# Kernel tuning notes

Measured on AMD Instinct MI355X. Metric: run time of the kernel, lower is better.

## Reference

```python
import jax, jax.numpy as jnp
import numpy as np

WS = (4, 4, 4)  # window shape (wd, wh, ww)
EPS = 1e-5


def _layernorm(x, g, b):
    mu = jnp.mean(x, axis=-1, keepdims=True)
    var = jnp.mean(jnp.square(x - mu), axis=-1, keepdims=True)
    return (x - mu) * jax.lax.rsqrt(var + EPS) * g + b


def _partition(x, ws):
    # x: [B, D, H, W, C] -> [num_windows, wd*wh*ww, C]
    B, D, H, W, C = x.shape
    x = x.reshape(B, D // ws[0], ws[0], H // ws[1], ws[1], W // ws[2], ws[2], C)
    x = jnp.transpose(x, (0, 1, 3, 5, 2, 4, 6, 7))
    return x.reshape(-1, ws[0] * ws[1] * ws[2], C)


def _merge(win, shape, ws):
    B, D, H, W, C = shape
    x = win.reshape(B, D // ws[0], H // ws[1], W // ws[2], ws[0], ws[1], ws[2], C)
    x = jnp.transpose(x, (0, 1, 4, 2, 5, 3, 6, 7))
    return x.reshape(B, D, H, W, C)


def setup_inputs() -> dict:
    key = jax.random.key(0)
    ks = jax.random.split(key, 8)
    B, D, H, W, C = 2, 32, 64, 64, 96
    nh, kd = 4, 24
    s = 0.02
    return {
        "x": jax.random.normal(ks[0], (B, D, H, W, C), jnp.float32),
        "ln1_g": jnp.ones((C,), jnp.float32),
        "ln1_b": jnp.zeros((C,), jnp.float32),
        "wq": jax.random.normal(ks[1], (C, nh, kd), jnp.float32) * s,
        "bq": jnp.zeros((nh, kd), jnp.float32),
        "wk": jax.random.normal(ks[2], (C, nh, kd), jnp.float32) * s,
        "bk": jnp.zeros((nh, kd), jnp.float32),
        "wv": jax.random.normal(ks[3], (C, nh, kd), jnp.float32) * s,
        "bv": jnp.zeros((nh, kd), jnp.float32),
        "wo": jax.random.normal(ks[4], (nh, kd, C), jnp.float32) * s,
        "bo": jnp.zeros((C,), jnp.float32),
        "ln2_g": jnp.ones((C,), jnp.float32),
        "ln2_b": jnp.zeros((C,), jnp.float32),
        "w1": jax.random.normal(ks[5], (C, 4 * C), jnp.float32) * s,
        "b1": jnp.zeros((4 * C,), jnp.float32),
        "w2": jax.random.normal(ks[6], (4 * C, C), jnp.float32) * s,
        "b2": jnp.zeros((C,), jnp.float32),
    }


def reference(x, ln1_g, ln1_b, wq, bq, wk, bk, wv, bv, wo, bo,
              ln2_g, ln2_b, w1, b1, w2, b2):
    shape = x.shape  # [B, D, H, W, C]; dims chosen divisible by WS -> pad is a no-op
    kd = wq.shape[-1]
    shortcut = x
    h = _layernorm(x, ln1_g, ln1_b)
    win = _partition(h, WS)  # [n, L, C], L = 64
    # Keras MultiHeadAttention (inference, dropout off)
    q = jnp.einsum("nlc,chd->nlhd", win, wq) + bq
    k = jnp.einsum("nlc,chd->nlhd", win, wk) + bk
    v = jnp.einsum("nlc,chd->nlhd", win, wv) + bv
    scores = jnp.einsum("nlhd,nmhd->nhlm", q, k) / jnp.sqrt(jnp.float32(kd))
    attn = jax.nn.softmax(scores, axis=-1)
    o = jnp.einsum("nhlm,nmhd->nlhd", attn, v)
    out = jnp.einsum("nlhd,hdc->nlc", o, wo) + bo
    x = shortcut + _merge(out, shape, WS)
    shortcut = x
    h = _layernorm(x, ln2_g, ln2_b)
    h = jax.nn.gelu(h @ w1 + b1, approximate=False)  # TF keras 'gelu' is exact
    h = h @ w2 + b2
    return shortcut + h
```

## Files before the change

kernel.cpp:

```cpp
#include <hip/hip_runtime.h>
#include <hip/hip_bf16.h>

typedef __attribute__((ext_vector_type(8))) short short8;
typedef __attribute__((ext_vector_type(4))) short short4b;
typedef __attribute__((ext_vector_type(4))) float f32x4;
typedef unsigned short ushort_t;

#define NTOK 262144

__device__ __forceinline__ ushort_t f2bf(float f){
  __hip_bfloat16 h = __float2bfloat16(f);
  return *reinterpret_cast<ushort_t*>(&h);
}
__device__ __forceinline__ float bf2f(ushort_t u){
  union { unsigned int i; float f; } v; v.i = ((unsigned int)u) << 16; return v.f;
}
__device__ __forceinline__ float fast_rcp(float x){
  float r; asm("v_rcp_f32 %0, %1" : "=v"(r) : "v"(x)); return r;
}
__device__ __forceinline__ float gelu_f(float x){
  float x2 = x * x;
  float z = x * fmaf(0.0356774081f, x2, 0.7978845608f);
  float e = __expf(2.0f * z);
  float t = 1.0f - 2.0f * fast_rcp(e + 1.0f);
  return 0.5f * x * (1.0f + t);
}
__device__ __forceinline__ void bar_lds(){
  asm volatile("s_waitcnt lgkmcnt(0)" ::: "memory");
  __builtin_amdgcn_s_barrier();
}
__device__ __forceinline__ void gl_lds16(const ushort_t* g, ushort_t* l){
  __builtin_amdgcn_global_load_lds(
      (const __attribute__((address_space(1))) void*)g,
      (__attribute__((address_space(3))) void*)l, 16, 0, 0);
}

template<int NT>
__device__ __forceinline__ void stage_w(const ushort_t* __restrict__ src,
                                        int src_stride, ushort_t (*dst)[104], int tid)
{
  #pragma unroll
  for (int it = 0; it < (1248 + NT - 1) / NT; ++it) {
    int u = tid + it * NT;
    if (u < 1248) {
      int row = u / 13, c16 = u % 13;
      const ushort_t* sp = src + row * src_stride + ((c16 == 12) ? 0 : c16 * 8);
      gl_lds16(sp, &dst[0][0] + (size_t)(u & ~63) * 8);
    }
  }
}

__global__ __launch_bounds__(256) void prep_kernel(
    const float* __restrict__ wq, const float* __restrict__ wk, const float* __restrict__ wv,
    const float* __restrict__ wo, const float* __restrict__ w1, const float* __restrict__ w2,
    const float* __restrict__ bq, const float* __restrict__ bk, const float* __restrict__ bv,
    ushort_t* __restrict__ Wqkv, ushort_t* __restrict__ Wo,
    ushort_t* __restrict__ W1, ushort_t* __restrict__ W2, float* __restrict__ biasq)
{
  const float qs = 0.20412414523193150818f;
  int i = blockIdx.x * 256 + threadIdx.x;
  if (i < 27648) {
    int j = i / 96, c = i % 96;
    int s = j / 96, rem = j % 96;
    const float* src = (s == 0) ? wq : (s == 1) ? wk : wv;
    float val = src[c * 96 + rem];
    if (s == 0) val *= qs;
    Wqkv[j * 96 + c] = f2bf(val);
  } else if (i < 36864) {
    int ii = i - 27648;
    int c = ii / 96, hd = ii % 96;
    Wo[ii] = f2bf(wo[hd * 96 + c]);
  } else if (i < 73728) {
    int ii = i - 36864;
    int j = ii / 96, c = ii % 96;
    W1[ii] = f2bf(w1[c * 384 + j]);
  } else if (i < 110592) {
    int ii = i - 73728;
    int c = ii / 384, j = ii % 384;
    W2[ii] = f2bf(w2[j * 96 + c]);
  } else if (i < 110880) {
    int j = i - 110592;
    int s = j / 96, rem = j % 96;
    const float* src = (s == 0) ? bq : (s == 1) ? bk : bv;
    float val = src[rem];
    if (s == 0) val *= qs;
    biasq[j] = val;
  }
}

__global__ __launch_bounds__(256, 2) void fat_kernel(
    const float* __restrict__ x, const float* __restrict__ g, const float* __restrict__ b,
    const ushort_t* __restrict__ Wqkv, const float* __restrict__ biasq,
    const ushort_t* __restrict__ Wo, const float* __restrict__ bo,
    ushort_t* __restrict__ x2b)
{
  __shared__ ushort_t regionA[19968];
  __shared__ ushort_t Vt[4][32][72];
  __shared__ ushort_t Ws[96][104];
  ushort_t (*hbt)[104]   = reinterpret_cast<ushort_t(*)[104]>(regionA);
  ushort_t (*QK)[208]    = reinterpret_cast<ushort_t(*)[208]>(regionA + 64 * 104);
  ushort_t (*Pb)[64][72] = reinterpret_cast<ushort_t(*)[64][72]>(regionA);
  ushort_t (*O_lds)[104] = reinterpret_cast<ushort_t(*)[104]>(regionA);

  int tid = threadIdx.x;
  int n = blockIdx.x;
  int wq_ = n & 15, hq = (n >> 4) & 15, rest = n >> 8;
  int dq = rest & 7, bb_ = rest >> 3;
  int base = bb_ * 131072 + dq * 16384 + hq * 256 + wq_ * 4;
  #define TOK(s) (base + ((s) >> 4) * 4096 + (((s) >> 2) & 3) * 64 + ((s) & 3))

  stage_w<256>(Wqkv, 96, Ws, tid);

  {
    int s = tid >> 2, qr = tid & 3;
    const float* xp = x + (size_t)TOK(s) * 96 + qr * 24;
    f32x4 v[6];
    float sm = 0.f, sq = 0.f;
    #pragma unroll
    for (int i = 0; i < 6; i++) {
      v[i] = *reinterpret_cast<const f32x4*>(xp + i * 4);
      #pragma unroll
      for (int j = 0; j < 4; j++) { sm += v[i][j]; sq += v[i][j] * v[i][j]; }
    }
    sm += __shfl_xor(sm, 1); sq += __shfl_xor(sq, 1);
    sm += __shfl_xor(sm, 2); sq += __shfl_xor(sq, 2);
    float mean = sm * (1.0f / 96.0f);
    float var  = sq * (1.0f / 96.0f) - mean * mean;
    float rstd = rsqrtf(var + 1e-5f);
    #pragma unroll
    for (int i8 = 0; i8 < 3; i8++) {
      short8 pk;
      #pragma unroll
      for (int j = 0; j < 8; j++) {
        int c = qr * 24 + i8 * 8 + j;
        pk[j] = (short)f2bf((v[(i8 * 8 + j) >> 2][(i8 * 8 + j) & 3] - mean) * rstd * g[c] + b[c]);
      }
      *reinterpret_cast<short8*>(&hbt[s][qr * 24 + i8 * 8]) = pk;
    }
  }
  __syncthreads();

  int w = tid >> 6, lane = tid & 63, g16 = lane >> 4, l15 = lane & 15;
  short8 af[3];
  #pragma unroll
  for (int ks = 0; ks < 3; ks++)
    af[ks] = *reinterpret_cast<const short8*>(&hbt[w * 16 + l15][ks * 32 + g16 * 8]);

  for (int grp = 0; grp < 3; ++grp) {
    f32x4 acc[6];
    #pragma unroll
    for (int j = 0; j < 6; j++) acc[j] = (f32x4){0.f, 0.f, 0.f, 0.f};
    #pragma unroll
    for (int j = 0; j < 6; j++)
      #pragma unroll
      for (int ks = 0; ks < 3; ks++) {
        short8 wfr = *reinterpret_cast<const short8*>(&Ws[j * 16 + l15][ks * 32 + g16 * 8]);
        acc[j] = __builtin_amdgcn_mfma_f32_16x16x32_bf16(wfr, af[ks], acc[j], 0, 0, 0);
      }
    bar_lds();
    if (grp < 2) stage_w<256>(Wqkv + (grp + 1) * 9216, 96, Ws, tid);
    else         stage_w<256>(Wo, 96, Ws, tid);
    if (grp < 2) {
      #pragma unroll
      for (int j = 0; j < 6; j++) {
        int c0 = grp * 96 + j * 16 + g16 * 4;
        f32x4 bb4 = *reinterpret_cast<const f32x4*>(&biasq[c0]);
        unsigned lo = (unsigned)f2bf(acc[j][0] + bb4[0]) | ((unsigned)f2bf(acc[j][1] + bb4[1]) << 16);
        unsigned hi = (unsigned)f2bf(acc[j][2] + bb4[2]) | ((unsigned)f2bf(acc[j][3] + bb4[3]) << 16);
        uint2 pk; pk.x = lo; pk.y = hi;
        *reinterpret_cast<uint2*>(&QK[w * 16 + l15][c0]) = pk;
      }
    } else {
      #pragma unroll
      for (int j = 0; j < 6; j++) {
        int c0 = j * 16 + g16 * 4;
        f32x4 bb4 = *reinterpret_cast<const f32x4*>(&biasq[192 + c0]);
        #pragma unroll
        for (int r = 0; r < 4; r++) {
          int vcol = c0 + r;
          int h2 = vcol / 24, d2 = vcol - h2 * 24;
          Vt[h2][d2][w * 16 + l15] = f2bf(acc[j][r] + bb4[r]);
        }
      }
    }
    __syncthreads();
  }

  int h = w;
  short8 kf[4], qf[4];
  const short8 z8 = {0, 0, 0, 0, 0, 0, 0, 0};
  #pragma unroll
  for (int i = 0; i < 4; i++) {
    qf[i] = (g16 < 3) ? *(const short8*)&QK[i * 16 + l15][h * 24 + g16 * 8]      : z8;
    kf[i] = (g16 < 3) ? *(const short8*)&QK[i * 16 + l15][96 + h * 24 + g16 * 8] : z8;
  }
  f32x4 st[4][4];
  #pragma unroll
  for (int tm = 0; tm < 4; tm++)
    #pragma unroll
    for (int tn = 0; tn < 4; tn++)
      st[tm][tn] = __builtin_amdgcn_mfma_f32_16x16x32_bf16(kf[tm], qf[tn],
                    (f32x4){0.f, 0.f, 0.f, 0.f}, 0, 0, 0);
  bar_lds();

  #pragma unroll
  for (int tn = 0; tn < 4; tn++) {
    float m = st[0][tn][0];
    #pragma unroll
    for (int tm = 0; tm < 4; tm++)
      #pragma unroll
      for (int r = 0; r < 4; r++) m = fmaxf(m, st[tm][tn][r]);
    m = fmaxf(m, __shfl_xor(m, 16));
    m = fmaxf(m, __shfl_xor(m, 32));
    float sum = 0.f;
    #pragma unroll
    for (int tm = 0; tm < 4; tm++)
      #pragma unroll
      for (int r = 0; r < 4; r++) {
        float e = __expf(st[tm][tn][r] - m);
        st[tm][tn][r] = e;
        sum += e;
      }
    sum += __shfl_xor(sum, 16);
    sum += __shfl_xor(sum, 32);
    float inv = fast_rcp(sum);
    int q = tn * 16 + l15;
    #pragma unroll
    for (int tm = 0; tm < 4; tm++) {
      unsigned lo = (unsigned)f2bf(st[tm][tn][0] * inv) | ((unsigned)f2bf(st[tm][tn][1] * inv) << 16);
      unsigned hi = (unsigned)f2bf(st[tm][tn][2] * inv) | ((unsigned)f2bf(st[tm][tn][3] * inv) << 16);
      uint2 pk; pk.x = lo; pk.y = hi;
      *(uint2*)&Pb[h][q][tm * 16 + g16 * 4] = pk;
    }
  }

  f32x4 oacc[4][2];
  #pragma unroll
  for (int qt = 0; qt < 4; qt++)
    #pragma unroll
    for (int dt = 0; dt < 2; dt++) oacc[qt][dt] = (f32x4){0.f, 0.f, 0.f, 0.f};
  #pragma unroll
  for (int ks = 0; ks < 2; ks++) {
    short8 vb[2];
    #pragma unroll
    for (int dt = 0; dt < 2; dt++)
      vb[dt] = *(const short8*)&Vt[h][dt * 16 + l15][ks * 32 + g16 * 8];
    #pragma unroll
    for (int qt = 0; qt < 4; qt++) {
      short8 pa = *(const short8*)&Pb[h][qt * 16 + l15][ks * 32 + g16 * 8];
      #pragma unroll
      for (int dt = 0; dt < 2; dt++)
        oacc[qt][dt] = __builtin_amdgcn_mfma_f32_16x16x32_bf16(pa, vb[dt], oacc[qt][dt], 0, 0, 0);
    }
  }

  __syncthreads();
  #pragma unroll
  for (int qt = 0; qt < 4; qt++)
    #pragma unroll
    for (int dt = 0; dt < 2; dt++) {
      int d = dt * 16 + l15;
      if (d < 24) {
        #pragma unroll
        for (int r = 0; r < 4; r++)
          O_lds[qt * 16 + g16 * 4 + r][h * 24 + d] = f2bf(oacc[qt][dt][r]);
      }
    }
  __syncthreads();

  f32x4 pacc[6];
  #pragma unroll
  for (int nt = 0; nt < 6; nt++) pacc[nt] = (f32x4){0.f, 0.f, 0.f, 0.f};
  #pragma unroll
  for (int ks = 0; ks < 3; ks++) {
    short8 pa = *(const short8*)&O_lds[w * 16 + l15][ks * 32 + g16 * 8];
    #pragma unroll
    for (int nt = 0; nt < 6; nt++) {
      short8 wb = *reinterpret_cast<const short8*>(&Ws[nt * 16 + l15][ks * 32 + g16 * 8]);
      pacc[nt] = __builtin_amdgcn_mfma_f32_16x16x32_bf16(pa, wb, pacc[nt], 0, 0, 0);
    }
  }
  #pragma unroll
  for (int nt = 0; nt < 6; nt++) {
    int col = nt * 16 + l15;
    float bs = bo[col];
    #pragma unroll
    for (int r = 0; r < 4; r++) {
      int s2 = w * 16 + g16 * 4 + r;
      size_t t = (size_t)TOK(s2);
      float v = pacc[nt][r] + bs + x[t * 96 + col];
      x2b[t * 96 + col] = f2bf(v);
    }
  }
  #undef TOK
}

__device__ __forceinline__ void ln_to_lds_b(const ushort_t* __restrict__ xrow_base,
    const float* __restrict__ gg, const float* __restrict__ bb,
    ushort_t (*hbt)[104], int tid)
{
  int row = tid >> 1, half = tid & 1;
  const ushort_t* xp = xrow_base + (size_t)row * 96 + half * 48;
  short8 vv[6];
  #pragma unroll
  for (int i = 0; i < 6; i++) vv[i] = *reinterpret_cast<const short8*>(xp + i * 8);
  float v[48];
  float s = 0.f, sq = 0.f;
  #pragma unroll
  for (int i = 0; i < 6; i++)
    #pragma unroll
    for (int j = 0; j < 8; j++) {
      float f = bf2f((ushort_t)vv[i][j]);
      v[i * 8 + j] = f; s += f; sq += f * f;
    }
  s  += __shfl_xor(s, 1);
  sq += __shfl_xor(sq, 1);
  float mean = s * (1.0f / 96.0f);
  float var  = sq * (1.0f / 96.0f) - mean * mean;
  float rstd = rsqrtf(var + 1e-5f);
  #pragma unroll
  for (int i8 = 0; i8 < 6; i8++) {
    short8 pk;
    #pragma unroll
    for (int j = 0; j < 8; j++) {
      int c = half * 48 + i8 * 8 + j;
      pk[j] = (short)f2bf((v[i8 * 8 + j] - mean) * rstd * gg[c] + bb[c]);
    }
    *reinterpret_cast<short8*>(&hbt[row][half * 48 + i8 * 8]) = pk;
  }
}

__global__ __launch_bounds__(256, 3) void mlp2_kernel(
    const ushort_t* __restrict__ x2b, const float* __restrict__ g, const float* __restrict__ b,
    const ushort_t* __restrict__ W1t, const float* __restrict__ b1,
    const ushort_t* __restrict__ W2t, const float* __restrict__ b2,
    float* __restrict__ out)
{
  __shared__ ushort_t smem[128][104];
  __shared__ ushort_t Ws[96][104];
  int tid = threadIdx.x;
  size_t r0 = (size_t)blockIdx.x * 128;

  stage_w<256>(W1t, 96, Ws, tid);
  ln_to_lds_b(x2b + r0 * 96, g, b, smem, tid);
  __syncthreads();

  int w = tid >> 6, lane = tid & 63, g16 = lane >> 4, l15 = lane & 15;
  short8 af[2][3];
  #pragma unroll
  for (int mi = 0; mi < 2; mi++)
    #pragma unroll
    for (int ks = 0; ks < 3; ks++)
      af[mi][ks] = *reinterpret_cast<const short8*>(&smem[w * 32 + mi * 16 + l15][ks * 32 + g16 * 8]);

  f32x4 oacc[6][2];
  #pragma unroll
  for (int nt = 0; nt < 6; nt++) { oacc[nt][0] = (f32x4){0.f,0.f,0.f,0.f}; oacc[nt][1] = (f32x4){0.f,0.f,0.f,0.f}; }

  for (int cc = 0; cc < 4; ++cc) {
    f32x4 acc[6][2];
    #pragma unroll
    for (int nt = 0; nt < 6; nt++) { acc[nt][0] = (f32x4){0.f,0.f,0.f,0.f}; acc[nt][1] = (f32x4){0.f,0.f,0.f,0.f}; }
    #pragma unroll
    for (int nt = 0; nt < 6; nt++)
      #pragma unroll
      for (int ks = 0; ks < 3; ks++) {
        short8 wfr = *reinterpret_cast<const short8*>(&Ws[nt * 16 + l15][ks * 32 + g16 * 8]);
        acc[nt][0] = __builtin_amdgcn_mfma_f32_16x16x32_bf16(wfr, af[0][ks], acc[nt][0], 0, 0, 0);
        acc[nt][1] = __builtin_amdgcn_mfma_f32_16x16x32_bf16(wfr, af[1][ks], acc[nt][1], 0, 0, 0);
      }
    bar_lds();
    stage_w<256>(W2t + cc * 96, 384, Ws, tid);
    #pragma unroll
    for (int nt = 0; nt < 6; nt++) {
      f32x4 bb4 = *reinterpret_cast<const f32x4*>(&b1[cc * 96 + nt * 16 + g16 * 4]);
      #pragma unroll
      for (int mi = 0; mi < 2; mi++) {
        float g0 = gelu_f(acc[nt][mi][0] + bb4[0]);
        float g1 = gelu_f(acc[nt][mi][1] + bb4[1]);
        float g2 = gelu_f(acc[nt][mi][2] + bb4[2]);
        float g3 = gelu_f(acc[nt][mi][3] + bb4[3]);
        unsigned lo = (unsigned)f2bf(g0) | ((unsigned)f2bf(g1) << 16);
        unsigned hi = (unsigned)f2bf(g2) | ((unsigned)f2bf(g3) << 16);
        uint2 pk; pk.x = lo; pk.y = hi;
        *reinterpret_cast<uint2*>(&smem[w * 32 + mi * 16 + l15][nt * 16 + g16 * 4]) = pk;
      }
    }
    short8 a2[2][3];
    #pragma unroll
    for (int mi = 0; mi < 2; mi++)
      #pragma unroll
      for (int ks = 0; ks < 3; ks++)
        a2[mi][ks] = *reinterpret_cast<const short8*>(&smem[w * 32 + mi * 16 + l15][ks * 32 + g16 * 8]);
    __syncthreads();
    #pragma unroll
    for (int nt = 0; nt < 6; nt++)
      #pragma unroll
      for (int ks = 0; ks < 3; ks++) {
        short8 wfr = *reinterpret_cast<const short8*>(&Ws[nt * 16 + l15][ks * 32 + g16 * 8]);
        oacc[nt][0] = __builtin_amdgcn_mfma_f32_16x16x32_bf16(wfr, a2[0][ks], oacc[nt][0], 0, 0, 0);
        oacc[nt][1] = __builtin_amdgcn_mfma_f32_16x16x32_bf16(wfr, a2[1][ks], oacc[nt][1], 0, 0, 0);
      }
    if (cc < 3) {
      bar_lds();
      stage_w<256>(W1t + (cc + 1) * 96 * 96, 96, Ws, tid);
      __syncthreads();
    }
  }

  #pragma unroll
  for (int nt = 0; nt < 6; nt++) {
    int c0 = nt * 16 + g16 * 4;
    f32x4 bb4 = *reinterpret_cast<const f32x4*>(&b2[c0]);
    #pragma unroll
    for (int mi = 0; mi < 2; mi++) {
      size_t row = r0 + w * 32 + mi * 16 + l15;
      short4b rr = *reinterpret_cast<const short4b*>(&x2b[row * 96 + c0]);
      f32x4 o;
      #pragma unroll
      for (int r = 0; r < 4; r++) o[r] = oacc[nt][mi][r] + bb4[r] + bf2f((ushort_t)rr[r]);
      *reinterpret_cast<f32x4*>(&out[row * 96 + c0]) = o;
    }
  }
}

extern "C" void kernel_launch(void* const* d_in, const int* in_sizes, int n_in,
                              void* d_out, int out_size, void* d_ws, size_t ws_size,
                              hipStream_t stream)
{
  (void)in_sizes; (void)n_in; (void)out_size; (void)ws_size;
  const float* x    = (const float*)d_in[0];
  const float* ln1g = (const float*)d_in[1];
  const float* ln1b = (const float*)d_in[2];
  const float* wq   = (const float*)d_in[3];
  const float* bq   = (const float*)d_in[4];
  const float* wk   = (const float*)d_in[5];
  const float* bk   = (const float*)d_in[6];
  const float* wv   = (const float*)d_in[7];
  const float* bv   = (const float*)d_in[8];
  const float* wo   = (const float*)d_in[9];
  const float* bo   = (const float*)d_in[10];
  const float* ln2g = (const float*)d_in[11];
  const float* ln2b = (const float*)d_in[12];
  const float* w1   = (const float*)d_in[13];
  const float* b1   = (const float*)d_in[14];
  const float* w2   = (const float*)d_in[15];
  const float* b2   = (const float*)d_in[16];

  char* ws = (char*)d_ws;
  ushort_t* x2b  = (ushort_t*)(ws);
  char* wsw      = ws + 50331648;
  ushort_t* Wqkv = (ushort_t*)(wsw);
  ushort_t* Wo   = (ushort_t*)(wsw + 55296);
  ushort_t* W1   = (ushort_t*)(wsw + 55296 + 18432);
  ushort_t* W2   = (ushort_t*)(wsw + 55296 + 18432 + 73728);
  float*    biasq= (float*)   (wsw + 55296 + 18432 + 73728 + 73728);

  prep_kernel<<<434, 256, 0, stream>>>(wq, wk, wv, wo, w1, w2, bq, bk, bv,
                                       Wqkv, Wo, W1, W2, biasq);
  fat_kernel<<<4096, 256, 0, stream>>>(x, ln1g, ln1b, Wqkv, biasq, Wo, bo, x2b);
  mlp2_kernel<<<NTOK / 128, 256, 0, stream>>>(x2b, ln2g, ln2b, W1, b1, W2, b2, (float*)d_out);
}
```

Measured before the change: 197.6 us.

## Double-buffer MLP weight tiles in LDS with vmcnt-based prefetch barriers

The MLP kernel now keeps separate LDS buffers for the W1 and W2 chunks and prefetches the next chunk with async global-to-LDS loads while the current GEMM runs. Barriers wait on partial vmcnt counts instead of draining all loads. Biases are staged in LDS, and the fat kernel's QK row stride is padded to 216. This aims to hide weight-load latency and cut barrier stalls, at the cost of more LDS, which lowers occupancy from 3 to 2 blocks per CU.

```diff
diff --git a/kernel.cpp b/kernel.cpp
--- a/kernel.cpp
+++ b/kernel.cpp
@@ -28,6 +28,17 @@
 __device__ __forceinline__ void bar_lds(){
   asm volatile("s_waitcnt lgkmcnt(0)" ::: "memory");
   __builtin_amdgcn_s_barrier();
+  __builtin_amdgcn_sched_barrier(0);
+}
+__device__ __forceinline__ void bar_cnt5(){
+  asm volatile("s_waitcnt vmcnt(5) lgkmcnt(0)" ::: "memory");
+  __builtin_amdgcn_s_barrier();
+  __builtin_amdgcn_sched_barrier(0);
+}
+__device__ __forceinline__ void bar_cnt0(){
+  asm volatile("s_waitcnt vmcnt(0) lgkmcnt(0)" ::: "memory");
+  __builtin_amdgcn_s_barrier();
+  __builtin_amdgcn_sched_barrier(0);
 }
 __device__ __forceinline__ void gl_lds16(const ushort_t* g, ushort_t* l){
   __builtin_amdgcn_global_load_lds(
@@ -47,6 +58,18 @@
       const ushort_t* sp = src + row * src_stride + ((c16 == 12) ? 0 : c16 * 8);
       gl_lds16(sp, &dst[0][0] + (size_t)(u & ~63) * 8);
     }
+  }
+}
+
+__device__ __forceinline__ void stage_wp(const ushort_t* __restrict__ src,
+                                         int src_stride, ushort_t* __restrict__ dst, int tid)
+{
+  #pragma unroll
+  for (int it = 0; it < 5; ++it) {
+    int u = tid + it * 256;
+    int row = u / 13, c16 = u % 13;
+    const ushort_t* sp = src + row * src_stride + ((c16 >= 12) ? 0 : c16 * 8);
+    gl_lds16(sp, dst + (size_t)(u & ~63) * 8);
   }
 }
 
@@ -94,11 +117,11 @@
     const ushort_t* __restrict__ Wo, const float* __restrict__ bo,
     ushort_t* __restrict__ x2b)
 {
-  __shared__ ushort_t regionA[19968];
+  __shared__ ushort_t regionA[20480];
   __shared__ ushort_t Vt[4][32][72];
   __shared__ ushort_t Ws[96][104];
   ushort_t (*hbt)[104]   = reinterpret_cast<ushort_t(*)[104]>(regionA);
-  ushort_t (*QK)[208]    = reinterpret_cast<ushort_t(*)[208]>(regionA + 64 * 104);
+  ushort_t (*QK)[216]    = reinterpret_cast<ushort_t(*)[216]>(regionA + 64 * 104);
   ushort_t (*Pb)[64][72] = reinterpret_cast<ushort_t(*)[64][72]>(regionA);
   ushort_t (*O_lds)[104] = reinterpret_cast<ushort_t(*)[104]>(regionA);
 
@@ -330,20 +353,26 @@
   }
 }
 
-__global__ __launch_bounds__(256, 3) void mlp2_kernel(
+__global__ __launch_bounds__(256, 2) void mlp2_kernel(
     const ushort_t* __restrict__ x2b, const float* __restrict__ g, const float* __restrict__ b,
     const ushort_t* __restrict__ W1t, const float* __restrict__ b1,
     const ushort_t* __restrict__ W2t, const float* __restrict__ b2,
     float* __restrict__ out)
 {
   __shared__ ushort_t smem[128][104];
-  __shared__ ushort_t Ws[96][104];
+  __shared__ ushort_t WsA[10240];
+  __shared__ ushort_t WsB[10240];
+  __shared__ float bias1[384];
+  __shared__ float bias2[96];
   int tid = threadIdx.x;
   size_t r0 = (size_t)blockIdx.x * 128;
 
-  stage_w<256>(W1t, 96, Ws, tid);
+  stage_wp(W1t, 96, WsA, tid);
+  stage_wp(W2t, 384, WsB, tid);
+  bias1[tid] = b1[tid];
+  if (tid < 128) bias1[256 + tid] = b1[256 + tid];
+  if (tid < 96)  bias2[tid] = b2[tid];
   ln_to_lds_b(x2b + r0 * 96, g, b, smem, tid);
-  __syncthreads();
 
   int w = tid >> 6, lane = tid & 63, g16 = lane >> 4, l15 = lane & 15;
   short8 af[2][3];
@@ -352,12 +381,14 @@
     #pragma unroll
     for (int ks = 0; ks < 3; ks++)
       af[mi][ks] = *reinterpret_cast<const short8*>(&smem[w * 32 + mi * 16 + l15][ks * 32 + g16 * 8]);
+  __builtin_amdgcn_sched_barrier(0);
 
   f32x4 oacc[6][2];
   #pragma unroll
   for (int nt = 0; nt < 6; nt++) { oacc[nt][0] = (f32x4){0.f,0.f,0.f,0.f}; oacc[nt][1] = (f32x4){0.f,0.f,0.f,0.f}; }
 
   for (int cc = 0; cc < 4; ++cc) {
+    bar_cnt5();
     f32x4 acc[6][2];
     #pragma unroll
     for (int nt = 0; nt < 6; nt++) { acc[nt][0] = (f32x4){0.f,0.f,0.f,0.f}; acc[nt][1] = (f32x4){0.f,0.f,0.f,0.f}; }
@@ -365,15 +396,13 @@
     for (int nt = 0; nt < 6; nt++)
       #pragma unroll
       for (int ks = 0; ks < 3; ks++) {
-        short8 wfr = *reinterpret_cast<const short8*>(&Ws[nt * 16 + l15][ks * 32 + g16 * 8]);
+        short8 wfr = *reinterpret_cast<const short8*>(&WsA[(nt * 16 + l15) * 104 + ks * 32 + g16 * 8]);
         acc[nt][0] = __builtin_amdgcn_mfma_f32_16x16x32_bf16(wfr, af[0][ks], acc[nt][0], 0, 0, 0);
         acc[nt][1] = __builtin_amdgcn_mfma_f32_16x16x32_bf16(wfr, af[1][ks], acc[nt][1], 0, 0, 0);
       }
-    bar_lds();
-    stage_w<256>(W2t + cc * 96, 384, Ws, tid);
     #pragma unroll
     for (int nt = 0; nt < 6; nt++) {
-      f32x4 bb4 = *reinterpret_cast<const f32x4*>(&b1[cc * 96 + nt * 16 + g16 * 4]);
+      f32x4 bb4 = *reinterpret_cast<const f32x4*>(&bias1[cc * 96 + nt * 16 + g16 * 4]);
       #pragma unroll
       for (int mi = 0; mi < 2; mi++) {
         float g0 = gelu_f(acc[nt][mi][0] + bb4[0]);
@@ -392,26 +421,27 @@
       #pragma unroll
       for (int ks = 0; ks < 3; ks++)
         a2[mi][ks] = *reinterpret_cast<const short8*>(&smem[w * 32 + mi * 16 + l15][ks * 32 + g16 * 8]);
-    __syncthreads();
+    bar_lds();
+    if (cc < 3) stage_wp(W1t + (cc + 1) * 9216, 96, WsA, tid);
+    if (cc < 3) bar_cnt5(); else bar_cnt0();
     #pragma unroll
     for (int nt = 0; nt < 6; nt++)
       #pragma unroll
       for (int ks = 0; ks < 3; ks++) {
-        short8 wfr = *reinterpret_cast<const short8*>(&Ws[nt * 16 + l15][ks * 32 + g16 * 8]);
+        short8 wfr = *reinterpret_cast<const short8*>(&WsB[(nt * 16 + l15) * 104 + ks * 32 + g16 * 8]);
         oacc[nt][0] = __builtin_amdgcn_mfma_f32_16x16x32_bf16(wfr, a2[0][ks], oacc[nt][0], 0, 0, 0);
         oacc[nt][1] = __builtin_amdgcn_mfma_f32_16x16x32_bf16(wfr, a2[1][ks], oacc[nt][1], 0, 0, 0);
       }
     if (cc < 3) {
       bar_lds();
-      stage_w<256>(W1t + (cc + 1) * 96 * 96, 96, Ws, tid);
-      __syncthreads();
+      stage_wp(W2t + (cc + 1) * 96, 384, WsB, tid);
     }
   }
 
   #pragma unroll
   for (int nt = 0; nt < 6; nt++) {
     int c0 = nt * 16 + g16 * 4;
-    f32x4 bb4 = *reinterpret_cast<const f32x4*>(&b2[c0]);
+    f32x4 bb4 = *reinterpret_cast<const f32x4*>(&bias2[c0]);
     #pragma unroll
     for (int mi = 0; mi < 2; mi++) {
       size_t row = r0 + w * 32 + mi * 16 + l15;
```

New measurement: 186.0 us. -5.9%, faster.
